# Kernel optimization log

Measured on AMD Instinct MI355X. Metric: run time of the kernel, lower is better.

## Reference

```python
import jax, jax.numpy as jnp
import numpy as np

N, D_IN, H, E, L = 8192, 512, 256, 262144, 2
LN_EPS = 1e-5


def _unique_edges(rng, n, e):
    # sample unique (src,tgt) pairs so scatter-set semantics are well-defined
    flat = np.unique(rng.integers(0, n * n, size=int(e * 1.2)))
    rng.shuffle(flat)
    flat = flat[:e]
    assert flat.shape[0] == e
    return np.stack([flat // n, flat % n]).astype(np.int64)


def setup_inputs() -> dict:
    key = jax.random.key(0)
    ks = jax.random.split(key, 8)
    rng = np.random.default_rng(0)
    inv = lambda fan: 1.0 / np.sqrt(fan)
    return {
        "node_features": jax.random.normal(ks[0], (N, D_IN), jnp.float32),
        "edge_index": jnp.asarray(_unique_edges(rng, N, E)),
        "W_in": jax.random.uniform(ks[1], (H, D_IN), jnp.float32, -inv(D_IN), inv(D_IN)),
        "b_in": jnp.zeros((H,), jnp.float32),
        "W_gat": jax.random.uniform(ks[2], (L, H, H), jnp.float32, -inv(H), inv(H)),
        "a_gat": jax.random.uniform(ks[3], (L, 2 * H), jnp.float32, -inv(2 * H), inv(2 * H)),
        "ln_g": jnp.ones((L, H), jnp.float32),
        "ln_b": jnp.zeros((L, H), jnp.float32),
        "W_pool": jax.random.uniform(ks[4], (1, H), jnp.float32, -inv(H), inv(H)),
        "b_pool": jnp.zeros((1,), jnp.float32),
    }


def _layer_norm(x, g, b):
    mu = x.mean(-1, keepdims=True)
    var = ((x - mu) ** 2).mean(-1, keepdims=True)
    return (x - mu) * jax.lax.rsqrt(var + LN_EPS) * g + b


def reference(node_features, edge_index, W_in, b_in, W_gat, a_gat, ln_g, ln_b, W_pool, b_pool):
    src, tgt = edge_index[0], edge_index[1]
    n = node_features.shape[0]
    h = node_features @ W_in.T + b_in  # (N, H)
    nl = W_gat.shape[0]
    for l in range(nl):
        hw = h @ W_gat[l].T  # (N, H)
        # attention score per edge: attn([h_src || h_tgt]) with LeakyReLU(0.2)
        e = hw[src] @ a_gat[l, :H] + hw[tgt] @ a_gat[l, H:]  # (E,)
        e = jnp.where(e > 0, e, 0.2 * e)
        # faithful to torch: dense NxN with zeros at non-edges, full-row softmax
        alpha = jnp.zeros((n, n), h.dtype).at[src, tgt].set(e)
        alpha = jax.nn.softmax(alpha, axis=-1)
        h_new = alpha @ hw  # (N, H)  (dropout is eval-mode identity)
        h = _layer_norm(h + h_new, ln_g[l], ln_b[l])
        h = jax.nn.elu(h)
    gate = jax.nn.sigmoid(h @ W_pool.T + b_pool)  # (N, 1)
    graph_emb = (gate * h).sum(axis=0)  # (H,)
    return h, graph_emb
```

## Files before the change

kernel.cpp:

```cpp
#include <hip/hip_runtime.h>
#include <hip/hip_bf16.h>
#include <stdint.h>

#define NN 8192
#define DIN 512
#define HH 256
#define EE 262144
#define CAP 96
#define LN_EPS 1e-5f

typedef __attribute__((ext_vector_type(8))) short bf16x8;
typedef __attribute__((ext_vector_type(4))) short s16x4;
typedef __attribute__((ext_vector_type(4))) float f32x4;

__device__ __forceinline__ short f2bf_bits(float x) {
    __hip_bfloat16 b = __float2bfloat16(x);
    return __builtin_bit_cast(short, b);
}
__device__ __forceinline__ float bf2f(short s) {
    uint32_t u = ((uint32_t)(uint16_t)s) << 16;
    return __builtin_bit_cast(float, u);
}
__device__ __forceinline__ void load16_lds(const void* g, void* l) {
    __builtin_amdgcn_global_load_lds((const __attribute__((address_space(1))) uint32_t*)g,
                                     (__attribute__((address_space(3))) uint32_t*)l, 16, 0, 0);
}

#define NW1 (HH * DIN)
#define NW2 (2 * HH * HH)
#define NX (NN * DIN)
#define ZCOUNT (2 * (2 * NN + HH) + NN)
__global__ __launch_bounds__(256) void prep(const float* __restrict__ W_in, __hip_bfloat16* __restrict__ Wb_in,
                                            const float* __restrict__ W_gat, __hip_bfloat16* __restrict__ Wgb,
                                            const float* __restrict__ X, __hip_bfloat16* __restrict__ Xb,
                                            float* __restrict__ zbase, float* __restrict__ emb) {
    int gtid = blockIdx.x * 256 + threadIdx.x;
    if (gtid < ZCOUNT) ((int*)zbase)[gtid] = 0;
    if (gtid < HH) emb[gtid] = 0.f;
    int q = gtid * 4;
    const float* x;
    __hip_bfloat16* y;
    int b;
    if (q < NW1) { x = W_in; y = Wb_in; b = q; }
    else if (q < NW1 + NW2) { x = W_gat; y = Wgb; b = q - NW1; }
    else if (q < NW1 + NW2 + NX) { x = X; y = Xb; b = q - NW1 - NW2; }
    else return;
    float4 v = *(const float4*)(x + b);
    y[b + 0] = __float2bfloat16(v.x);
    y[b + 1] = __float2bfloat16(v.y);
    y[b + 2] = __float2bfloat16(v.z);
    y[b + 3] = __float2bfloat16(v.w);
}

__global__ void fill_buckets(const int* __restrict__ src, const int* __restrict__ tgt,
                             int* __restrict__ cnt, int* __restrict__ buck) {
    int k = blockIdx.x * 256 + threadIdx.x;
    if (k < EE) {
        int s = src[k];
        int p = atomicAdd(&cnt[s], 1);
        if (p < CAP) buck[s * CAP + p] = tgt[k];
    }
}

__global__ __launch_bounds__(256) void gemm_bb_bias(const __hip_bfloat16* __restrict__ A,
                                                    const __hip_bfloat16* __restrict__ B,
                                                    const float* __restrict__ bias,
                                                    __hip_bfloat16* __restrict__ Cb,
                                                    int Nc, int K) {
    __shared__ __hip_bfloat16 As[64 * 32];
    __shared__ __hip_bfloat16 Bs[64 * 32];
    const int tid = threadIdx.x;
    const int row0 = blockIdx.y * 64, col0 = blockIdx.x * 64;
    const int w = tid >> 6, l = tid & 63;
    const int quad = l >> 4, r = l & 15;
    const int mh = (w & 1) * 32, nh = (w >> 1) * 32;
    f32x4 acc[2][2] = {};

    const int srow = tid >> 2, scol = (tid & 3) * 8;
    const __hip_bfloat16* gA = A + (size_t)(row0 + srow) * K + scol;
    const __hip_bfloat16* gB = B + (size_t)(col0 + srow) * K + scol;
    __hip_bfloat16* lA = &As[tid * 8];
    __hip_bfloat16* lB = &Bs[tid * 8];

    for (int k0 = 0; k0 < K; k0 += 32) {
        load16_lds(gA + k0, lA);
        load16_lds(gB + k0, lB);
        __syncthreads();
        bf16x8 aF[2], bF[2];
#pragma unroll
        for (int mi = 0; mi < 2; mi++)
            aF[mi] = *(const bf16x8*)&As[(mh + mi * 16 + r) * 32 + quad * 8];
#pragma unroll
        for (int ni = 0; ni < 2; ni++)
            bF[ni] = *(const bf16x8*)&Bs[(nh + ni * 16 + r) * 32 + quad * 8];
#pragma unroll
        for (int mi = 0; mi < 2; mi++)
#pragma unroll
            for (int ni = 0; ni < 2; ni++)
                acc[mi][ni] = __builtin_amdgcn_mfma_f32_16x16x32_bf16(aF[mi], bF[ni], acc[mi][ni], 0, 0, 0);
        __syncthreads();
    }

#pragma unroll
    for (int mi = 0; mi < 2; mi++)
#pragma unroll
        for (int ni = 0; ni < 2; ni++) {
            int gcol = col0 + nh + ni * 16 + r;
            float bv = bias[gcol];
#pragma unroll
            for (int reg = 0; reg < 4; reg++) {
                int grow = row0 + mh + mi * 16 + quad * 4 + reg;
                Cb[(size_t)grow * Nc + gcol] = __float2bfloat16(acc[mi][ni][reg] + bv);
            }
        }
}

__global__ __launch_bounds__(256) void gemm_bb_score(const __hip_bfloat16* __restrict__ A,
                                                     const __hip_bfloat16* __restrict__ B,
                                                     __hip_bfloat16* __restrict__ Cb,
                                                     const float* __restrict__ ag1,
                                                     const float* __restrict__ ag2,
                                                     float* __restrict__ s1, float* __restrict__ s2,
                                                     float* __restrict__ St,
                                                     int Nc, int K) {
    __shared__ __hip_bfloat16 As[64 * 32];
    __shared__ __hip_bfloat16 Bs[64 * 32];
    const int tid = threadIdx.x;
    const int row0 = blockIdx.y * 64, col0 = blockIdx.x * 64;
    const int w = tid >> 6, l = tid & 63;
    const int quad = l >> 4, r = l & 15;
    const int mh = (w & 1) * 32, nh = (w >> 1) * 32;
    f32x4 acc[2][2] = {};

    const int srow = tid >> 2, scol = (tid & 3) * 8;
    const __hip_bfloat16* gA = A + (size_t)(row0 + srow) * K + scol;
    const __hip_bfloat16* gB = B + (size_t)(col0 + srow) * K + scol;
    __hip_bfloat16* lA = &As[tid * 8];
    __hip_bfloat16* lB = &Bs[tid * 8];

    for (int k0 = 0; k0 < K; k0 += 32) {
        load16_lds(gA + k0, lA);
        load16_lds(gB + k0, lB);
        __syncthreads();
        bf16x8 aF[2], bF[2];
#pragma unroll
        for (int mi = 0; mi < 2; mi++)
            aF[mi] = *(const bf16x8*)&As[(mh + mi * 16 + r) * 32 + quad * 8];
#pragma unroll
        for (int ni = 0; ni < 2; ni++)
            bF[ni] = *(const bf16x8*)&Bs[(nh + ni * 16 + r) * 32 + quad * 8];
#pragma unroll
        for (int mi = 0; mi < 2; mi++)
#pragma unroll
            for (int ni = 0; ni < 2; ni++)
                acc[mi][ni] = __builtin_amdgcn_mfma_f32_16x16x32_bf16(aF[mi], bF[ni], acc[mi][ni], 0, 0, 0);
        __syncthreads();
    }

#pragma unroll
    for (int mi = 0; mi < 2; mi++)
#pragma unroll
        for (int ni = 0; ni < 2; ni++) {
            int gcol = col0 + nh + ni * 16 + r;
#pragma unroll
            for (int reg = 0; reg < 4; reg++) {
                int grow = row0 + mh + mi * 16 + quad * 4 + reg;
                Cb[(size_t)grow * Nc + gcol] = __float2bfloat16(acc[mi][ni][reg]);
            }
        }

    float a1v[2], a2v[2];
#pragma unroll
    for (int ni = 0; ni < 2; ni++) {
        int gcol = col0 + nh + ni * 16 + r;
        a1v[ni] = ag1[gcol];
        a2v[ni] = ag2[gcol];
    }
#pragma unroll
    for (int mi = 0; mi < 2; mi++)
#pragma unroll
        for (int reg = 0; reg < 4; reg++) {
            float p1 = acc[mi][0][reg] * a1v[0] + acc[mi][1][reg] * a1v[1];
            float p2 = acc[mi][0][reg] * a2v[0] + acc[mi][1][reg] * a2v[1];
#pragma unroll
            for (int off = 1; off <= 8; off <<= 1) {
                p1 += __shfl_xor(p1, off);
                p2 += __shfl_xor(p2, off);
            }
            if (r == 0) {
                int grow = row0 + mh + mi * 16 + quad * 4 + reg;
                atomicAdd(&s1[grow], p1);
                atomicAdd(&s2[grow], p2);
            }
        }
#pragma unroll
    for (int ni = 0; ni < 2; ni++) {
        float pS = 0.f;
#pragma unroll
        for (int mi = 0; mi < 2; mi++)
#pragma unroll
            for (int reg = 0; reg < 4; reg++) pS += acc[mi][ni][reg];
        pS += __shfl_xor(pS, 16);
        pS += __shfl_xor(pS, 32);
        if (quad == 0) atomicAdd(&St[col0 + nh + ni * 16 + r], pS);
    }
}

__global__ __launch_bounds__(256) void gat_row(const __hip_bfloat16* __restrict__ hprev,
                                               const __hip_bfloat16* __restrict__ hw,
                                               const int* __restrict__ cnt, const int* __restrict__ buck,
                                               const float* __restrict__ s1, const float* __restrict__ s2,
                                               const float* __restrict__ St,
                                               const float* __restrict__ lng, const float* __restrict__ lnb,
                                               const float* __restrict__ W_pool, const float* __restrict__ b_pool,
                                               float* __restrict__ houtf, __hip_bfloat16* __restrict__ houtb,
                                               float* __restrict__ gate, int last) {
    const int wv = threadIdx.x >> 6, lane = threadIdx.x & 63;
    const int i = blockIdx.x * 4 + wv;
    const int deg = cnt[i];
    const int base = i * CAP;
    const float s1i = s1[i];
    const short* hws = (const short*)hw;

    float u0 = 0.f, u1 = 0.f, u2 = 0.f, u3 = 0.f;
    float lsum = 0.f;

    for (int kb = 0; kb < deg; kb += 64) {
        int k = kb + lane;
        float wk = 0.f;
        int ck = 0;
        if (k < deg) {
            int j = buck[base + k];
            float e = s1i + s2[j];
            e = e > 0.f ? e : 0.2f * e;
            wk = __expf(e) - 1.f;
            ck = j;
        }
        lsum += wk;
        int nb = min(64, deg - kb);
#pragma unroll 4
        for (int jj = 0; jj < nb; jj++) {
            float wj = __shfl(wk, jj);
            int cj = __shfl(ck, jj);
            s16x4 hv = *(const s16x4*)(hws + (size_t)cj * HH + 4 * lane);
            u0 += wj * bf2f(hv[0]);
            u1 += wj * bf2f(hv[1]);
            u2 += wj * bf2f(hv[2]);
            u3 += wj * bf2f(hv[3]);
        }
    }
#pragma unroll
    for (int off = 32; off; off >>= 1) lsum += __shfl_xor(lsum, off);
    const float inv = 1.f / ((float)NN + lsum);

    const float4 Stv = *(const float4*)(St + 4 * lane);
    s16x4 hp = *(const s16x4*)((const short*)hprev + (size_t)i * HH + 4 * lane);
    float x0 = bf2f(hp[0]) + (Stv.x + u0) * inv;
    float x1 = bf2f(hp[1]) + (Stv.y + u1) * inv;
    float x2 = bf2f(hp[2]) + (Stv.z + u2) * inv;
    float x3 = bf2f(hp[3]) + (Stv.w + u3) * inv;
    float ssum = x0 + x1 + x2 + x3;
#pragma unroll
    for (int off = 32; off; off >>= 1) ssum += __shfl_xor(ssum, off);
    float mu = ssum * (1.f / HH);
    float d0 = x0 - mu, d1 = x1 - mu, d2 = x2 - mu, d3 = x3 - mu;
    float vsum = d0 * d0 + d1 * d1 + d2 * d2 + d3 * d3;
#pragma unroll
    for (int off = 32; off; off >>= 1) vsum += __shfl_xor(vsum, off);
    float rstd = rsqrtf(vsum * (1.f / HH) + LN_EPS);
    float4 g4 = *(const float4*)(lng + 4 * lane);
    float4 b4 = *(const float4*)(lnb + 4 * lane);
    float y0 = d0 * rstd * g4.x + b4.x;
    float y1 = d1 * rstd * g4.y + b4.y;
    float y2 = d2 * rstd * g4.z + b4.z;
    float y3 = d3 * rstd * g4.w + b4.w;
    y0 = y0 > 0.f ? y0 : __expf(y0) - 1.f;
    y1 = y1 > 0.f ? y1 : __expf(y1) - 1.f;
    y2 = y2 > 0.f ? y2 : __expf(y2) - 1.f;
    y3 = y3 > 0.f ? y3 : __expf(y3) - 1.f;

    s16x4 yv;
    yv[0] = f2bf_bits(y0); yv[1] = f2bf_bits(y1); yv[2] = f2bf_bits(y2); yv[3] = f2bf_bits(y3);
    *(s16x4*)((short*)houtb + (size_t)i * HH + 4 * lane) = yv;
    if (houtf) {
        float4 yf = { y0, y1, y2, y3 };
        *(float4*)(houtf + (size_t)i * HH + 4 * lane) = yf;
    }

    if (last) {
        float4 wp = *(const float4*)(W_pool + 4 * lane);
        float p = y0 * wp.x + y1 * wp.y + y2 * wp.z + y3 * wp.w;
#pragma unroll
        for (int off = 32; off; off >>= 1) p += __shfl_xor(p, off);
        if (lane == 0) {
            float g = p + b_pool[0];
            gate[i] = 1.f / (1.f + __expf(-g));
        }
    }
}

__global__ __launch_bounds__(256) void pool_kernel(const float* __restrict__ h, const float* __restrict__ gate,
                                                   float* __restrict__ emb) {
    int c = threadIdx.x;
    int r0 = blockIdx.x * 32;
    float acc = 0.f;
#pragma unroll
    for (int rr = 0; rr < 32; rr++) {
        int r = r0 + rr;
        acc += gate[r] * h[(size_t)r * HH + c];
    }
    atomicAdd(&emb[c], acc);
}

extern "C" void kernel_launch(void* const* d_in, const int* in_sizes, int n_in,
                              void* d_out, int out_size, void* d_ws, size_t ws_size,
                              hipStream_t stream) {
    const float* X      = (const float*)d_in[0];
    const int*   ei     = (const int*)d_in[1];
    const float* W_in   = (const float*)d_in[2];
    const float* b_in   = (const float*)d_in[3];
    const float* W_gat  = (const float*)d_in[4];
    const float* a_gat  = (const float*)d_in[5];
    const float* ln_g   = (const float*)d_in[6];
    const float* ln_b   = (const float*)d_in[7];
    const float* W_pool = (const float*)d_in[8];
    const float* b_pool = (const float*)d_in[9];
    float* out = (float*)d_out;

    __hip_bfloat16* hb    = (__hip_bfloat16*)d_ws;
    __hip_bfloat16* hwb   = hb + (size_t)NN * HH;
    __hip_bfloat16* Wb_in = hwb + (size_t)NN * HH;
    __hip_bfloat16* Wgb   = Wb_in + (size_t)HH * DIN;
    __hip_bfloat16* Xb    = Wgb + (size_t)2 * HH * HH;
    float* zbase = (float*)(Xb + (size_t)NN * DIN);
    float* s1_0 = zbase;
    float* s2_0 = s1_0 + NN;
    float* St_0 = s2_0 + NN;
    float* s1_1 = St_0 + HH;
    float* s2_1 = s1_1 + NN;
    float* St_1 = s2_1 + NN;
    int* cnt  = (int*)(St_1 + HH);
    float* gate = (float*)(cnt + NN);
    int* buck = (int*)(gate + NN);

    const int* src = ei;
    const int* tgt = ei + EE;
    float* emb = out + (size_t)NN * HH;

    int prep_quads = (NW1 + NW2 + NX) / 4;
    prep<<<(prep_quads + 255) / 256, 256, 0, stream>>>(W_in, Wb_in, W_gat, Wgb, X, Xb, zbase, emb);

    fill_buckets<<<EE / 256, 256, 0, stream>>>(src, tgt, cnt, buck);

    gemm_bb_bias<<<dim3(HH / 64, NN / 64), 256, 0, stream>>>(Xb, Wb_in, b_in, hb, HH, DIN);

    for (int ll = 0; ll < 2; ll++) {
        float* s1 = ll ? s1_1 : s1_0;
        float* s2 = ll ? s2_1 : s2_0;
        float* St = ll ? St_1 : St_0;
        const float* ag = a_gat + (size_t)ll * 2 * HH;
        gemm_bb_score<<<dim3(HH / 64, NN / 64), 256, 0, stream>>>(hb, Wgb + (size_t)ll * HH * HH, hwb,
                                                                  ag, ag + HH, s1, s2, St, HH, HH);
        gat_row<<<NN / 4, 256, 0, stream>>>(hb, hwb, cnt, buck, s1, s2, St,
                                            ln_g + (size_t)ll * HH, ln_b + (size_t)ll * HH,
                                            W_pool, b_pool,
                                            (ll == 1) ? out : nullptr, hb, gate, ll);
    }

    pool_kernel<<<NN / 32, 256, 0, stream>>>(out, gate, emb);
}
```

Measured before the change: 183.4 us.

## Fuse gated pooling into last GAT layer and vectorize edge bucketing

The separate pool kernel is removed. The last gat_row launch computes the sigmoid gate per row, combines the four rows of each block through shared memory, and atomically adds the partial sums into the embedding. The bf16 copy of h is no longer written on the last layer, and fill_buckets handles two edges per thread using int2 loads. This saves one launch and a reread of the float h output, at the cost of more atomics on the 256-element embedding (one per block instead of one per 32 rows).

```diff
diff --git a/kernel.cpp b/kernel.cpp
--- a/kernel.cpp
+++ b/kernel.cpp
@@ -54,11 +54,14 @@
 
 __global__ void fill_buckets(const int* __restrict__ src, const int* __restrict__ tgt,
                              int* __restrict__ cnt, int* __restrict__ buck) {
-    int k = blockIdx.x * 256 + threadIdx.x;
+    int k = (blockIdx.x * 256 + threadIdx.x) * 2;
     if (k < EE) {
-        int s = src[k];
-        int p = atomicAdd(&cnt[s], 1);
-        if (p < CAP) buck[s * CAP + p] = tgt[k];
+        int2 sv = *(const int2*)(src + k);
+        int2 tv = *(const int2*)(tgt + k);
+        int p = atomicAdd(&cnt[sv.x], 1);
+        if (p < CAP) buck[sv.x * CAP + p] = tv.x;
+        p = atomicAdd(&cnt[sv.y], 1);
+        if (p < CAP) buck[sv.y * CAP + p] = tv.y;
     }
 }
 
@@ -214,7 +217,8 @@
                                                const float* __restrict__ lng, const float* __restrict__ lnb,
                                                const float* __restrict__ W_pool, const float* __restrict__ b_pool,
                                                float* __restrict__ houtf, __hip_bfloat16* __restrict__ houtb,
-                                               float* __restrict__ gate, int last) {
+                                               float* __restrict__ emb, int last) {
+    __shared__ float sAcc[4][HH];
     const int wv = threadIdx.x >> 6, lane = threadIdx.x & 63;
     const int i = blockIdx.x * 4 + wv;
     const int deg = cnt[i];
@@ -279,9 +283,11 @@
     y2 = y2 > 0.f ? y2 : __expf(y2) - 1.f;
     y3 = y3 > 0.f ? y3 : __expf(y3) - 1.f;
 
-    s16x4 yv;
-    yv[0] = f2bf_bits(y0); yv[1] = f2bf_bits(y1); yv[2] = f2bf_bits(y2); yv[3] = f2bf_bits(y3);
-    *(s16x4*)((short*)houtb + (size_t)i * HH + 4 * lane) = yv;
+    if (houtb) {
+        s16x4 yv;
+        yv[0] = f2bf_bits(y0); yv[1] = f2bf_bits(y1); yv[2] = f2bf_bits(y2); yv[3] = f2bf_bits(y3);
+        *(s16x4*)((short*)houtb + (size_t)i * HH + 4 * lane) = yv;
+    }
     if (houtf) {
         float4 yf = { y0, y1, y2, y3 };
         *(float4*)(houtf + (size_t)i * HH + 4 * lane) = yf;
@@ -292,24 +298,16 @@
         float p = y0 * wp.x + y1 * wp.y + y2 * wp.z + y3 * wp.w;
 #pragma unroll
         for (int off = 32; off; off >>= 1) p += __shfl_xor(p, off);
-        if (lane == 0) {
-            float g = p + b_pool[0];
-            gate[i] = 1.f / (1.f + __expf(-g));
-        }
-    }
-}
-
-__global__ __launch_bounds__(256) void pool_kernel(const float* __restrict__ h, const float* __restrict__ gate,
-                                                   float* __restrict__ emb) {
-    int c = threadIdx.x;
-    int r0 = blockIdx.x * 32;
-    float acc = 0.f;
-#pragma unroll
-    for (int rr = 0; rr < 32; rr++) {
-        int r = r0 + rr;
-        acc += gate[r] * h[(size_t)r * HH + c];
-    }
-    atomicAdd(&emb[c], acc);
+        float g = 1.f / (1.f + __expf(-(p + b_pool[0])));
+        sAcc[wv][4 * lane + 0] = g * y0;
+        sAcc[wv][4 * lane + 1] = g * y1;
+        sAcc[wv][4 * lane + 2] = g * y2;
+        sAcc[wv][4 * lane + 3] = g * y3;
+        __syncthreads();
+        int t = threadIdx.x;
+        float part = sAcc[0][t] + sAcc[1][t] + sAcc[2][t] + sAcc[3][t];
+        atomicAdd(&emb[t], part);
+    }
 }
 
 extern "C" void kernel_launch(void* const* d_in, const int* in_sizes, int n_in,
@@ -340,8 +338,7 @@
     float* s2_1 = s1_1 + NN;
     float* St_1 = s2_1 + NN;
     int* cnt  = (int*)(St_1 + HH);
-    float* gate = (float*)(cnt + NN);
-    int* buck = (int*)(gate + NN);
+    int* buck = cnt + NN;
 
     const int* src = ei;
     const int* tgt = ei + EE;
@@ -350,7 +347,7 @@
     int prep_quads = (NW1 + NW2 + NX) / 4;
     prep<<<(prep_quads + 255) / 256, 256, 0, stream>>>(W_in, Wb_in, W_gat, Wgb, X, Xb, zbase, emb);
 
-    fill_buckets<<<EE / 256, 256, 0, stream>>>(src, tgt, cnt, buck);
+    fill_buckets<<<EE / 512, 256, 0, stream>>>(src, tgt, cnt, buck);
 
     gemm_bb_bias<<<dim3(HH / 64, NN / 64), 256, 0, stream>>>(Xb, Wb_in, b_in, hb, HH, DIN);
 
@@ -364,8 +361,8 @@
         gat_row<<<NN / 4, 256, 0, stream>>>(hb, hwb, cnt, buck, s1, s2, St,
                                             ln_g + (size_t)ll * HH, ln_b + (size_t)ll * HH,
                                             W_pool, b_pool,
-                                            (ll == 1) ? out : nullptr, hb, gate, ll);
-    }
-
-    pool_kernel<<<NN / 32, 256, 0, stream>>>(out, gate, emb);
-}
+                                            (ll == 1) ? out : nullptr,
+                                            (ll == 0) ? hb : nullptr,
+                                            emb, ll);
+    }
+}
```

Result: slower. 221.2 us (+20.6%).
